# Performance work log

Measured on AMD Instinct MI355X. Metric: run time of the kernel, lower is better.

## Reference

```python
import jax, jax.numpy as jnp
import numpy as np

N, E, D, H = 100000, 1600000, 32, 32


def setup_inputs() -> dict:
    key = jax.random.key(0)
    k1, k2, k3, k4 = jax.random.split(key, 4)
    x = jax.random.normal(k1, (N, D), dtype=jnp.float32)
    edge_index = jax.random.randint(k2, (2, E), 0, N, dtype=jnp.int64)
    W1 = jax.random.normal(k3, (D, H), dtype=jnp.float32) * (1.0 / np.sqrt(D))
    b1 = jnp.zeros((H,), dtype=jnp.float32)
    W2 = jax.random.normal(k4, (H, H), dtype=jnp.float32) * (1.0 / np.sqrt(H))
    b2 = jnp.zeros((H,), dtype=jnp.float32)
    return {"x": x, "edge_index": edge_index, "W1": W1, "b1": b1, "W2": W2, "b2": b2}


def _gcn_conv(x, src, dst, norm, W, b, n_nodes):
    # h = x W  ->  gather at src, scale by sym-norm, scatter-add at dst, + bias
    h = x @ W                                   # [N, H]
    msg = h[src] * norm[:, None]                # [E+N, H]
    out = jax.ops.segment_sum(msg, dst, num_segments=n_nodes)
    return out + b


def reference(x, edge_index, W1, b1, W2, b2):
    n = x.shape[0]
    loops = jnp.arange(n, dtype=edge_index.dtype)
    src = jnp.concatenate([edge_index[0], loops])  # source nodes (+ self loops)
    dst = jnp.concatenate([edge_index[1], loops])  # target nodes (+ self loops)
    # symmetric normalization: deg^{-1/2}[src] * deg^{-1/2}[dst] on A + I
    deg = jax.ops.segment_sum(jnp.ones_like(dst, dtype=x.dtype), dst, num_segments=n)
    dis = jnp.where(deg > 0, jax.lax.rsqrt(jnp.maximum(deg, 1e-12)), 0.0)
    norm = dis[src] * dis[dst]
    # layer 1: GCNConv -> ReLU (dropout is identity in eval mode)
    h = jax.nn.relu(_gcn_conv(x, src, dst, norm, W1, b1, n))
    # layer 2
    h = jax.nn.relu(_gcn_conv(h, src, dst, norm, W2, b2, n))
    return h
```

## Files before the change

kernel.cpp:

```cpp
#include <hip/hip_runtime.h>
#include <hip/hip_fp16.h>

#define FEAT 32
#define BIN_NODES 128
#define BIN_SHIFT 7
#define TILE_EDGES 8192
#define BWAVES 16
#define SRC_BITS 20
#define SRC_MASK 0xFFFFF
#define STAGE_CAP 6144

__device__ __forceinline__ int block_detect_int64(const int* __restrict__ raw32, int* nz) {
    if (threadIdx.x == 0) *nz = 0;
    __syncthreads();
    if (raw32[2 * threadIdx.x + 1] != 0) *nz = 1;
    __syncthreads();
    return (*nz == 0) ? 1 : 0;
}

__device__ __forceinline__ int load_idx(const void* raw, int f, long long i) {
    return f ? (int)((const long long*)raw)[i] : ((const int*)raw)[i];
}

__global__ __launch_bounds__(1024)
void binA_kernel(const void* __restrict__ raw, int* __restrict__ mat,
                 int* __restrict__ bin_tot, int e, int nb) {
    extern __shared__ int hist[];
    int t = threadIdx.x;
    for (int i = t; i < BWAVES * nb; i += 1024) hist[i] = 0;
    int f = block_detect_int64((const int*)raw, &hist[BWAVES * nb]);
    int w = t >> 6, lane = t & 63;
    long long base = (long long)blockIdx.x * TILE_EDGES;
    int cnt = (int)min((long long)TILE_EDGES, (long long)e - base);
    int* hw = hist + w * nb;
    const int seg = TILE_EDGES / BWAVES;
    int wbeg = w * seg;
    int wend = min(wbeg + seg, cnt);
    for (int i = wbeg + lane; i < wend; i += 64) {
        int d = load_idx(raw, f, (long long)e + base + i);
        atomicAdd(&hw[d >> BIN_SHIFT], 1);
    }
    __syncthreads();
    for (int b = t; b < nb; b += 1024) {
        int s = 0;
#pragma unroll
        for (int w2 = 0; w2 < BWAVES; ++w2) s += hist[w2 * nb + b];
        mat[blockIdx.x * nb + b] = s;
        if (s) atomicAdd(&bin_tot[b], s);
    }
}

__global__ __launch_bounds__(1024)
void scanb_kernel(const int* __restrict__ bin_tot, int* __restrict__ bin_base,
                  int* __restrict__ cursor, int nb, int e) {
    __shared__ int sd[1024];
    int t = threadIdx.x;
    int v = (t < nb) ? bin_tot[t] : 0;
    sd[t] = v;
    __syncthreads();
    for (int off = 1; off < 1024; off <<= 1) {
        int add = (t >= off) ? sd[t - off] : 0;
        __syncthreads();
        sd[t] += add;
        __syncthreads();
    }
    if (t < nb) {
        int ex = sd[t] - v;
        bin_base[t] = ex;
        cursor[t] = ex;
    }
    if (t == nb) bin_base[nb] = e;
}

__global__ __launch_bounds__(1024)
void binC_kernel(const void* __restrict__ raw, const int* __restrict__ mat,
                 int* __restrict__ cursor, int* __restrict__ packed,
                 int e, int nb) {
    extern __shared__ int cur[];
    int t = threadIdx.x;
    int f = block_detect_int64((const int*)raw, &cur[nb]);
    for (int i = t; i < nb; i += 1024) {
        int c = mat[blockIdx.x * nb + i];
        cur[i] = c ? atomicAdd(&cursor[i], c) : 0;
    }
    __syncthreads();
    long long base = (long long)blockIdx.x * TILE_EDGES;
    int cnt = (int)min((long long)TILE_EDGES, (long long)e - base);
    for (int i = t; i < cnt; i += 1024) {
        long long ei = base + i;
        int s = load_idx(raw, f, ei);
        int d = load_idx(raw, f, (long long)e + ei);
        int b = d >> BIN_SHIFT;
        int pos = atomicAdd(&cur[b], 1);
        packed[pos] = s | ((d & (BIN_NODES - 1)) << SRC_BITS);
    }
}

__global__ __launch_bounds__(1024)
void degsort_kernel(const int* __restrict__ packed, const int* __restrict__ bin_base,
                    float* __restrict__ dis, int* __restrict__ row_start,
                    int* __restrict__ recs, const float* __restrict__ x,
                    const float* __restrict__ W1, __half* __restrict__ h1,
                    int e, int n, int nb) {
    __shared__ int cnt[BWAVES][BIN_NODES];
    __shared__ int wcur[BWAVES][BIN_NODES];
    __shared__ int exc[BIN_NODES];
    __shared__ float sdis[BIN_NODES];
    __shared__ float W1l[FEAT * FEAT];
    __shared__ int stage[STAGE_CAP];
    int b = blockIdx.x, t = threadIdx.x;
    int w = t >> 6;
    for (int i = t; i < BWAVES * BIN_NODES; i += 1024) ((int*)cnt)[i] = 0;
    if (t < FEAT * FEAT) W1l[t] = W1[t];
    __syncthreads();
    int start = bin_base[b];
    int end = bin_base[b + 1];
    int m = end - start;
    if (m <= STAGE_CAP) {
        for (int i = t; i < m; i += 1024) {
            int rec = packed[start + i];
            stage[i] = rec;
            atomicAdd(&cnt[w][rec >> SRC_BITS], 1);
        }
    } else {
        for (int i = start + t; i < end; i += 1024)
            atomicAdd(&cnt[w][packed[i] >> SRC_BITS], 1);
    }
    __syncthreads();
    if (t < BIN_NODES) {
        int s = 0;
#pragma unroll
        for (int w2 = 0; w2 < BWAVES; ++w2) s += cnt[w2][t];
        exc[t] = s;
    }
    __syncthreads();
    for (int off = 1; off < BIN_NODES; off <<= 1) {
        int v = 0;
        if (t < BIN_NODES && t >= off) v = exc[t - off];
        __syncthreads();
        if (t < BIN_NODES) exc[t] += v;
        __syncthreads();
    }
    if (t < BIN_NODES) {
        int tot = 0;
#pragma unroll
        for (int w2 = 0; w2 < BWAVES; ++w2) tot += cnt[w2][t];
        int rs = start + exc[t] - tot;
        int run = rs;
#pragma unroll
        for (int w2 = 0; w2 < BWAVES; ++w2) { wcur[w2][t] = run; run += cnt[w2][t]; }
        float dv = rsqrtf((float)tot + 1.0f);
        sdis[t] = dv;
        int node = b * BIN_NODES + t;
        if (node < n) {
            dis[node] = dv;
            row_start[node] = rs;
        }
    }
    if (b == 0 && t == 128) row_start[n] = e;
    __syncthreads();
    if (m <= STAGE_CAP) {
        for (int i = t; i < m; i += 1024) {
            int rec = stage[i];
            int pos = atomicAdd(&wcur[w][rec >> SRC_BITS], 1);
            recs[pos] = rec & SRC_MASK;
        }
    } else {
        for (int i = start + t; i < end; i += 1024) {
            int rec = packed[i];
            int pos = atomicAdd(&wcur[w][rec >> SRC_BITS], 1);
            recs[pos] = rec & SRC_MASK;
        }
    }
    {
        int ln = b * BIN_NODES + (t >> 3);
        if (ln < n) {
            int q = t & 7;
            float4 xv = ((const float4*)x)[(size_t)ln * 8 + q];
            float xr[4] = {xv.x, xv.y, xv.z, xv.w};
            float o[4] = {0.f, 0.f, 0.f, 0.f};
#pragma unroll
            for (int k = 0; k < FEAT; ++k) {
                float xk = __shfl(xr[k & 3], k >> 2, 8);
#pragma unroll
                for (int c = 0; c < 4; ++c)
                    o[c] = fmaf(xk, W1l[k * FEAT + q * 4 + c], o[c]);
            }
            float dn = sdis[t >> 3];
            __half2* hp = (__half2*)&h1[(size_t)ln * FEAT + q * 4];
            hp[0] = __halves2half2(__float2half(dn * o[0]), __float2half(dn * o[1]));
            hp[1] = __halves2half2(__float2half(dn * o[2]), __float2half(dn * o[3]));
        }
    }
}

__global__ __launch_bounds__(256, 8)
void pull_mm_kernel(const int* __restrict__ recs, const int* __restrict__ row_start,
                    const __half* __restrict__ h, const float* __restrict__ dis,
                    const float* __restrict__ bias, const float* __restrict__ W2,
                    __half* __restrict__ h2, int n) {
    __shared__ float Wl[FEAT * FEAT];
    int t = threadIdx.x;
    for (int i = t; i < FEAT * FEAT; i += 256) {
        int k = i >> 5, j = i & 31;
        int col = (j & 24) | ((j + 2 * (k >> 3)) & 7);
        Wl[k * FEAT + col] = W2[i];
    }
    __syncthreads();
    int node = blockIdx.x * 16 + (t >> 4);
    if (node >= n) return;
    int g = t & 15;
    int sub = g >> 2;
    int fb = g & 3;
    int start = row_start[node];
    int deg = row_start[node + 1] - start;
    const float4* h4 = (const float4*)h;
    float s0 = 0, s1 = 0, s2 = 0, s3 = 0, s4 = 0, s5 = 0, s6 = 0, s7 = 0;
    for (int r0 = 0; r0 < deg; r0 += 32) {
#pragma unroll
        for (int w = 0; w < 8; ++w) {
            int r = r0 + w * 4 + sub;
            if (r < deg) {
                int s = recs[start + r];
                float4 v = h4[(size_t)s * 4 + fb];
                const __half2* hp = (const __half2*)&v;
                float2 a = __half22float2(hp[0]);
                float2 b = __half22float2(hp[1]);
                float2 c = __half22float2(hp[2]);
                float2 d = __half22float2(hp[3]);
                s0 += a.x; s1 += a.y; s2 += b.x; s3 += b.y;
                s4 += c.x; s5 += c.y; s6 += d.x; s7 += d.y;
            }
        }
    }
#pragma unroll
    for (int m = 4; m <= 8; m <<= 1) {
        s0 += __shfl_xor(s0, m, 64); s1 += __shfl_xor(s1, m, 64);
        s2 += __shfl_xor(s2, m, 64); s3 += __shfl_xor(s3, m, 64);
        s4 += __shfl_xor(s4, m, 64); s5 += __shfl_xor(s5, m, 64);
        s6 += __shfl_xor(s6, m, 64); s7 += __shfl_xor(s7, m, 64);
    }
    float dn = dis[node];
    float4 hv = h4[(size_t)node * 4 + fb];
    const __half2* hp = (const __half2*)&hv;
    float2 a = __half22float2(hp[0]);
    float2 b = __half22float2(hp[1]);
    float2 c = __half22float2(hp[2]);
    float2 d = __half22float2(hp[3]);
    const float4* bv4 = (const float4*)bias;
    float4 b0 = bv4[fb * 2], b1 = bv4[fb * 2 + 1];
    float o[8];
    o[0] = fmaxf(fmaf(dn, s0 + a.x, b0.x), 0.0f);
    o[1] = fmaxf(fmaf(dn, s1 + a.y, b0.y), 0.0f);
    o[2] = fmaxf(fmaf(dn, s2 + b.x, b0.z), 0.0f);
    o[3] = fmaxf(fmaf(dn, s3 + b.y, b0.w), 0.0f);
    o[4] = fmaxf(fmaf(dn, s4 + c.x, b1.x), 0.0f);
    o[5] = fmaxf(fmaf(dn, s5 + c.y, b1.y), 0.0f);
    o[6] = fmaxf(fmaf(dn, s6 + d.x, b1.z), 0.0f);
    o[7] = fmaxf(fmaf(dn, s7 + d.y, b1.w), 0.0f);
    float part[8] = {0.f, 0.f, 0.f, 0.f, 0.f, 0.f, 0.f, 0.f};
    const float* wrow = &Wl[(fb * 8) * FEAT + sub * 8];
#pragma unroll
    for (int cc = 0; cc < 8; ++cc) {
#pragma unroll
        for (int c2 = 0; c2 < 8; ++c2)
            part[c2] = fmaf(o[cc], wrow[cc * FEAT + ((c2 + 2 * fb) & 7)], part[c2]);
    }
#pragma unroll
    for (int m = 1; m <= 2; m <<= 1) {
        part[0] += __shfl_xor(part[0], m, 64); part[1] += __shfl_xor(part[1], m, 64);
        part[2] += __shfl_xor(part[2], m, 64); part[3] += __shfl_xor(part[3], m, 64);
        part[4] += __shfl_xor(part[4], m, 64); part[5] += __shfl_xor(part[5], m, 64);
        part[6] += __shfl_xor(part[6], m, 64); part[7] += __shfl_xor(part[7], m, 64);
    }
    if (fb == 0) {
        __half2 p0 = __halves2half2(__float2half(dn * part[0]), __float2half(dn * part[1]));
        __half2 p1 = __halves2half2(__float2half(dn * part[2]), __float2half(dn * part[3]));
        __half2 p2 = __halves2half2(__float2half(dn * part[4]), __float2half(dn * part[5]));
        __half2 p3 = __halves2half2(__float2half(dn * part[6]), __float2half(dn * part[7]));
        float4 pk;
        ((__half2*)&pk)[0] = p0; ((__half2*)&pk)[1] = p1;
        ((__half2*)&pk)[2] = p2; ((__half2*)&pk)[3] = p3;
        ((float4*)h2)[(size_t)node * 4 + sub] = pk;
    }
}

__global__ __launch_bounds__(256, 8)
void pull_kernel(const int* __restrict__ recs, const int* __restrict__ row_start,
                 const __half* __restrict__ h, const float* __restrict__ dis,
                 const float* __restrict__ bias, float* __restrict__ out, int n) {
    int t = threadIdx.x;
    int node = blockIdx.x * 16 + (t >> 4);
    if (node >= n) return;
    int g = t & 15;
    int sub = g >> 2;
    int fb = g & 3;
    int start = row_start[node];
    int deg = row_start[node + 1] - start;
    const float4* h4 = (const float4*)h;
    float s0 = 0, s1 = 0, s2 = 0, s3 = 0, s4 = 0, s5 = 0, s6 = 0, s7 = 0;
    for (int r0 = 0; r0 < deg; r0 += 32) {
#pragma unroll
        for (int w = 0; w < 8; ++w) {
            int r = r0 + w * 4 + sub;
            if (r < deg) {
                int s = recs[start + r];
                float4 v = h4[(size_t)s * 4 + fb];
                const __half2* hp = (const __half2*)&v;
                float2 a = __half22float2(hp[0]);
                float2 b = __half22float2(hp[1]);
                float2 c = __half22float2(hp[2]);
                float2 d = __half22float2(hp[3]);
                s0 += a.x; s1 += a.y; s2 += b.x; s3 += b.y;
                s4 += c.x; s5 += c.y; s6 += d.x; s7 += d.y;
            }
        }
    }
#pragma unroll
    for (int m = 4; m <= 8; m <<= 1) {
        s0 += __shfl_xor(s0, m, 64); s1 += __shfl_xor(s1, m, 64);
        s2 += __shfl_xor(s2, m, 64); s3 += __shfl_xor(s3, m, 64);
        s4 += __shfl_xor(s4, m, 64); s5 += __shfl_xor(s5, m, 64);
        s6 += __shfl_xor(s6, m, 64); s7 += __shfl_xor(s7, m, 64);
    }
    if (sub == 0) {
        float dn = dis[node];
        float4 hv = h4[(size_t)node * 4 + fb];
        const __half2* hp = (const __half2*)&hv;
        float2 a = __half22float2(hp[0]);
        float2 b = __half22float2(hp[1]);
        float2 c = __half22float2(hp[2]);
        float2 d = __half22float2(hp[3]);
        const float4* bv4 = (const float4*)bias;
        float4 b0 = bv4[fb * 2], b1 = bv4[fb * 2 + 1];
        float4 o0, o1;
        o0.x = fmaxf(fmaf(dn, s0 + a.x, b0.x), 0.0f);
        o0.y = fmaxf(fmaf(dn, s1 + a.y, b0.y), 0.0f);
        o0.z = fmaxf(fmaf(dn, s2 + b.x, b0.z), 0.0f);
        o0.w = fmaxf(fmaf(dn, s3 + b.y, b0.w), 0.0f);
        o1.x = fmaxf(fmaf(dn, s4 + c.x, b1.x), 0.0f);
        o1.y = fmaxf(fmaf(dn, s5 + c.y, b1.y), 0.0f);
        o1.z = fmaxf(fmaf(dn, s6 + d.x, b1.z), 0.0f);
        o1.w = fmaxf(fmaf(dn, s7 + d.y, b1.w), 0.0f);
        ((float4*)out)[(size_t)node * 8 + fb * 2] = o0;
        ((float4*)out)[(size_t)node * 8 + fb * 2 + 1] = o1;
    }
}

extern "C" void kernel_launch(void* const* d_in, const int* in_sizes, int n_in,
                              void* d_out, int out_size, void* d_ws, size_t ws_size,
                              hipStream_t stream) {
    const float* x = (const float*)d_in[0];
    const void* eidx_raw = d_in[1];
    const float* W1 = (const float*)d_in[2];
    const float* b1 = (const float*)d_in[3];
    const float* W2 = (const float*)d_in[4];
    const float* b2 = (const float*)d_in[5];
    float* out = (float*)d_out;

    const int n = in_sizes[0] / FEAT;
    const int e = in_sizes[1] / 2;
    const int nb = (n + BIN_NODES - 1) / BIN_NODES;
    const int nblk = (e + TILE_EDGES - 1) / TILE_EDGES;
    const int M = nb * nblk;

    char* ws = (char*)d_ws;
    size_t off = 0;
    auto alloc = [&](size_t bytes) { char* p = ws + off; off = (off + bytes + 255) & ~(size_t)255; return p; };
    int*    mat       = (int*)   alloc((size_t)M * 4);
    int*    bin_tot   = (int*)   alloc((size_t)nb * 4);
    int*    bin_base  = (int*)   alloc((size_t)(nb + 1) * 4);
    int*    cursor    = (int*)   alloc((size_t)nb * 4);
    float*  dis       = (float*) alloc((size_t)n * 4);
    int*    row_start = (int*)   alloc((size_t)(n + 1) * 4);
    int*    recs      = (int*)   alloc((size_t)e * 4);
    __half* h1        = (__half*)alloc((size_t)n * FEAT * 2);
    __half* h2        = (__half*)alloc((size_t)(n * FEAT * 2 > e * 4 ? (size_t)n * FEAT * 2 : (size_t)e * 4));
    int*    packed    = (int*)h2;

    const size_t ldsA = (size_t)(BWAVES * nb + 1) * 4;
    const size_t ldsC = (size_t)(nb + 1) * 4;
    const int gNode = (n + 15) / 16;

    hipMemsetAsync(bin_tot, 0, (size_t)nb * 4, stream);
    binA_kernel<<<nblk, 1024, ldsA, stream>>>(eidx_raw, mat, bin_tot, e, nb);
    scanb_kernel<<<1, 1024, 0, stream>>>(bin_tot, bin_base, cursor, nb, e);
    binC_kernel<<<nblk, 1024, ldsC, stream>>>(eidx_raw, mat, cursor, packed, e, nb);
    degsort_kernel<<<nb, 1024, 0, stream>>>(packed, bin_base, dis, row_start,
                                            recs, x, W1, h1, e, n, nb);

    pull_mm_kernel<<<gNode, 256, 0, stream>>>(recs, row_start, h1, dis, b1, W2, h2, n);
    pull_kernel<<<gNode, 256, 0, stream>>>(recs, row_start, h2, dis, b2, out, n);
}
```

Before: 187.4 us.

## Fuse edge histogram and scatter into one pass using fixed-capacity bin slots

```diff
diff --git a/kernel.cpp b/kernel.cpp
--- a/kernel.cpp
+++ b/kernel.cpp
@@ -6,56 +6,75 @@
 #define BIN_SHIFT 7
 #define TILE_EDGES 8192
 #define BWAVES 16
+#define NC 8
 #define SRC_BITS 20
 #define SRC_MASK 0xFFFFF
 #define STAGE_CAP 6144
 
-__device__ __forceinline__ int block_detect_int64(const int* __restrict__ raw32, int* nz) {
-    if (threadIdx.x == 0) *nz = 0;
-    __syncthreads();
-    if (raw32[2 * threadIdx.x + 1] != 0) *nz = 1;
-    __syncthreads();
-    return (*nz == 0) ? 1 : 0;
-}
-
 __device__ __forceinline__ int load_idx(const void* raw, int f, long long i) {
     return f ? (int)((const long long*)raw)[i] : ((const int*)raw)[i];
 }
 
 __global__ __launch_bounds__(1024)
-void binA_kernel(const void* __restrict__ raw, int* __restrict__ mat,
-                 int* __restrict__ bin_tot, int e, int nb) {
-    extern __shared__ int hist[];
-    int t = threadIdx.x;
-    for (int i = t; i < BWAVES * nb; i += 1024) hist[i] = 0;
-    int f = block_detect_int64((const int*)raw, &hist[BWAVES * nb]);
-    int w = t >> 6, lane = t & 63;
+void initc_kernel(int* __restrict__ cursor, int nb, int cap) {
+    int t = threadIdx.x;
+    if (t < nb) cursor[t] = t * cap;
+}
+
+__global__ __launch_bounds__(1024)
+void binAC_kernel(const void* __restrict__ raw, int* __restrict__ cursor,
+                  int* __restrict__ packed, int e, int nb) {
+    extern __shared__ int lds[];
+    int t = threadIdx.x;
+    int* hist = lds;
+    int* cur  = lds + NC * nb;
+    int* nz   = lds + NC * nb + nb;
+    for (int i = t; i < NC * nb; i += 1024) hist[i] = 0;
+    if (t == 0) *nz = 0;
+    __syncthreads();
+    if (((const int*)raw)[2 * t + 1] != 0) *nz = 1;
+    __syncthreads();
+    const int f = (*nz == 0) ? 1 : 0;
+
     long long base = (long long)blockIdx.x * TILE_EDGES;
     int cnt = (int)min((long long)TILE_EDGES, (long long)e - base);
-    int* hw = hist + w * nb;
-    const int seg = TILE_EDGES / BWAVES;
-    int wbeg = w * seg;
-    int wend = min(wbeg + seg, cnt);
-    for (int i = wbeg + lane; i < wend; i += 64) {
-        int d = load_idx(raw, f, (long long)e + base + i);
-        atomicAdd(&hw[d >> BIN_SHIFT], 1);
+    int sreg[8], dreg[8];
+    int* hw = hist + ((t >> 6) & (NC - 1)) * nb;
+#pragma unroll
+    for (int k = 0; k < 8; ++k) {
+        int i = t + k * 1024;
+        if (i < cnt) {
+            sreg[k] = load_idx(raw, f, base + i);
+            dreg[k] = load_idx(raw, f, (long long)e + base + i);
+            atomicAdd(&hw[dreg[k] >> BIN_SHIFT], 1);
+        } else {
+            dreg[k] = -1;
+        }
     }
     __syncthreads();
     for (int b = t; b < nb; b += 1024) {
         int s = 0;
 #pragma unroll
-        for (int w2 = 0; w2 < BWAVES; ++w2) s += hist[w2 * nb + b];
-        mat[blockIdx.x * nb + b] = s;
-        if (s) atomicAdd(&bin_tot[b], s);
+        for (int c = 0; c < NC; ++c) s += hist[c * nb + b];
+        cur[b] = s ? atomicAdd(&cursor[b], s) : 0;
+    }
+    __syncthreads();
+#pragma unroll
+    for (int k = 0; k < 8; ++k) {
+        int d = dreg[k];
+        if (d >= 0) {
+            int pos = atomicAdd(&cur[d >> BIN_SHIFT], 1);
+            packed[pos] = sreg[k] | ((d & (BIN_NODES - 1)) << SRC_BITS);
+        }
     }
 }
 
 __global__ __launch_bounds__(1024)
-void scanb_kernel(const int* __restrict__ bin_tot, int* __restrict__ bin_base,
-                  int* __restrict__ cursor, int nb, int e) {
+void scanb_kernel(const int* __restrict__ cursor, int* __restrict__ bin_base,
+                  int nb, int cap, int e) {
     __shared__ int sd[1024];
     int t = threadIdx.x;
-    int v = (t < nb) ? bin_tot[t] : 0;
+    int v = (t < nb) ? (cursor[t] - t * cap) : 0;
     sd[t] = v;
     __syncthreads();
     for (int off = 1; off < 1024; off <<= 1) {
@@ -64,36 +83,8 @@
         sd[t] += add;
         __syncthreads();
     }
-    if (t < nb) {
-        int ex = sd[t] - v;
-        bin_base[t] = ex;
-        cursor[t] = ex;
-    }
+    if (t < nb) bin_base[t] = sd[t] - v;
     if (t == nb) bin_base[nb] = e;
-}
-
-__global__ __launch_bounds__(1024)
-void binC_kernel(const void* __restrict__ raw, const int* __restrict__ mat,
-                 int* __restrict__ cursor, int* __restrict__ packed,
-                 int e, int nb) {
-    extern __shared__ int cur[];
-    int t = threadIdx.x;
-    int f = block_detect_int64((const int*)raw, &cur[nb]);
-    for (int i = t; i < nb; i += 1024) {
-        int c = mat[blockIdx.x * nb + i];
-        cur[i] = c ? atomicAdd(&cursor[i], c) : 0;
-    }
-    __syncthreads();
-    long long base = (long long)blockIdx.x * TILE_EDGES;
-    int cnt = (int)min((long long)TILE_EDGES, (long long)e - base);
-    for (int i = t; i < cnt; i += 1024) {
-        long long ei = base + i;
-        int s = load_idx(raw, f, ei);
-        int d = load_idx(raw, f, (long long)e + ei);
-        int b = d >> BIN_SHIFT;
-        int pos = atomicAdd(&cur[b], 1);
-        packed[pos] = s | ((d & (BIN_NODES - 1)) << SRC_BITS);
-    }
 }
 
 __global__ __launch_bounds__(1024)
@@ -101,7 +92,7 @@
                     float* __restrict__ dis, int* __restrict__ row_start,
                     int* __restrict__ recs, const float* __restrict__ x,
                     const float* __restrict__ W1, __half* __restrict__ h1,
-                    int e, int n, int nb) {
+                    int e, int n, int nb, int cap) {
     __shared__ int cnt[BWAVES][BIN_NODES];
     __shared__ int wcur[BWAVES][BIN_NODES];
     __shared__ int exc[BIN_NODES];
@@ -114,17 +105,17 @@
     if (t < FEAT * FEAT) W1l[t] = W1[t];
     __syncthreads();
     int start = bin_base[b];
-    int end = bin_base[b + 1];
-    int m = end - start;
+    int m = bin_base[b + 1] - start;
+    long long pbase = (long long)b * cap;
     if (m <= STAGE_CAP) {
         for (int i = t; i < m; i += 1024) {
-            int rec = packed[start + i];
+            int rec = packed[pbase + i];
             stage[i] = rec;
             atomicAdd(&cnt[w][rec >> SRC_BITS], 1);
         }
     } else {
-        for (int i = start + t; i < end; i += 1024)
-            atomicAdd(&cnt[w][packed[i] >> SRC_BITS], 1);
+        for (int i = t; i < m; i += 1024)
+            atomicAdd(&cnt[w][packed[pbase + i] >> SRC_BITS], 1);
     }
     __syncthreads();
     if (t < BIN_NODES) {
@@ -166,8 +157,8 @@
             recs[pos] = rec & SRC_MASK;
         }
     } else {
-        for (int i = start + t; i < end; i += 1024) {
-            int rec = packed[i];
+        for (int i = t; i < m; i += 1024) {
+            int rec = packed[pbase + i];
             int pos = atomicAdd(&wcur[w][rec >> SRC_BITS], 1);
             recs[pos] = rec & SRC_MASK;
         }
@@ -362,32 +353,31 @@
     const int e = in_sizes[1] / 2;
     const int nb = (n + BIN_NODES - 1) / BIN_NODES;
     const int nblk = (e + TILE_EDGES - 1) / TILE_EDGES;
-    const int M = nb * nblk;
+    const int avg = (e + nb - 1) / nb;
+    const int cap = (avg + (avg >> 1) + 255) & ~255;
 
     char* ws = (char*)d_ws;
     size_t off = 0;
     auto alloc = [&](size_t bytes) { char* p = ws + off; off = (off + bytes + 255) & ~(size_t)255; return p; };
-    int*    mat       = (int*)   alloc((size_t)M * 4);
-    int*    bin_tot   = (int*)   alloc((size_t)nb * 4);
+    int*    cursor    = (int*)   alloc((size_t)nb * 4);
     int*    bin_base  = (int*)   alloc((size_t)(nb + 1) * 4);
-    int*    cursor    = (int*)   alloc((size_t)nb * 4);
     float*  dis       = (float*) alloc((size_t)n * 4);
     int*    row_start = (int*)   alloc((size_t)(n + 1) * 4);
     int*    recs      = (int*)   alloc((size_t)e * 4);
     __half* h1        = (__half*)alloc((size_t)n * FEAT * 2);
-    __half* h2        = (__half*)alloc((size_t)(n * FEAT * 2 > e * 4 ? (size_t)n * FEAT * 2 : (size_t)e * 4));
+    size_t  packed_bytes = (size_t)nb * cap * 4;
+    size_t  h2_bytes     = (size_t)n * FEAT * 2;
+    __half* h2        = (__half*)alloc(packed_bytes > h2_bytes ? packed_bytes : h2_bytes);
     int*    packed    = (int*)h2;
 
-    const size_t ldsA = (size_t)(BWAVES * nb + 1) * 4;
-    const size_t ldsC = (size_t)(nb + 1) * 4;
+    const size_t ldsAC = (size_t)(NC * nb + nb + 1) * 4;
     const int gNode = (n + 15) / 16;
 
-    hipMemsetAsync(bin_tot, 0, (size_t)nb * 4, stream);
-    binA_kernel<<<nblk, 1024, ldsA, stream>>>(eidx_raw, mat, bin_tot, e, nb);
-    scanb_kernel<<<1, 1024, 0, stream>>>(bin_tot, bin_base, cursor, nb, e);
-    binC_kernel<<<nblk, 1024, ldsC, stream>>>(eidx_raw, mat, cursor, packed, e, nb);
+    initc_kernel<<<1, 1024, 0, stream>>>(cursor, nb, cap);
+    binAC_kernel<<<nblk, 1024, ldsAC, stream>>>(eidx_raw, cursor, packed, e, nb);
+    scanb_kernel<<<1, 1024, 0, stream>>>(cursor, bin_base, nb, cap, e);
     degsort_kernel<<<nb, 1024, 0, stream>>>(packed, bin_base, dis, row_start,
-                                            recs, x, W1, h1, e, n, nb);
+                                            recs, x, W1, h1, e, n, nb, cap);
 
     pull_mm_kernel<<<gNode, 256, 0, stream>>>(recs, row_start, h1, dis, b1, W2, h2, n);
     pull_kernel<<<gNode, 256, 0, stream>>>(recs, row_start, h2, dis, b2, out, n);
```

Result: faster. 177.4 us (-5.3%).
